# Kernel optimization log

Measured on AMD Instinct MI355X. Metric: run time of the kernel, lower is better.

The kernel has to match this reference:

```python
import jax, jax.numpy as jnp
import numpy as np
from jax import lax

NUM_SELECT = 300
TGT_H, TGT_W = 512, 512  # static resize target; all target_sizes entries equal this


def box_cxcywh_to_xyxy(b):
    cx, cy, w, h = jnp.split(b, 4, axis=-1)
    return jnp.concatenate([cx - 0.5 * w, cy - 0.5 * h, cx + 0.5 * w, cy + 0.5 * h], axis=-1)


def setup_inputs() -> dict:
    key = jax.random.key(0)
    k1, k2, k3, k4 = jax.random.split(key, 4)
    B, Q, C, D, mh, mw = 2, 900, 91, 4, 128, 128
    return {
        "pred_logits": jax.random.normal(k1, (B, Q, C), dtype=jnp.float32),
        "pred_boxes": jax.random.uniform(k2, (B, Q, 4), dtype=jnp.float32),
        "pred_masks": jax.random.normal(k3, (B, Q, mh, mw), dtype=jnp.float32),
        "pred_log_vars": jax.random.normal(k4, (B, Q, D), dtype=jnp.float32),
        "target_sizes": jnp.full((B, 2), TGT_H, dtype=jnp.int32),
    }


def reference(pred_logits, pred_boxes, pred_masks, pred_log_vars, target_sizes):
    B, Q, C = pred_logits.shape
    prob = jax.nn.sigmoid(pred_logits)                      # [B,Q,C]
    topk_values, topk_indexes = lax.top_k(prob.reshape(B, Q * C), NUM_SELECT)
    scores = topk_values                                     # [B,K]
    topk_boxes = topk_indexes // C                           # [B,K] query index
    labels = topk_indexes % C                                # [B,K]

    boxes = box_cxcywh_to_xyxy(pred_boxes)                   # [B,Q,4]
    boxes = jnp.take_along_axis(boxes, topk_boxes[:, :, None], axis=1)  # [B,K,4]

    glv = jnp.take_along_axis(pred_log_vars, topk_boxes[:, :, None], axis=1)  # [B,K,D]
    uncertainty = glv.mean(axis=-1)                          # [B,K]

    ts = target_sizes.astype(boxes.dtype)
    img_h, img_w = ts[:, 0], ts[:, 1]
    scale_fct = jnp.stack([img_w, img_h, img_w, img_h], axis=1)  # [B,4]
    boxes = boxes * scale_fct[:, None, :]

    # gather masks for selected queries, then bilinear resize (align_corners=False)
    sel_masks = jnp.take_along_axis(
        pred_masks, topk_boxes[:, :, None, None], axis=1)    # [B,K,mh,mw]
    mask_logits = jax.image.resize(
        sel_masks, (B, NUM_SELECT, TGT_H, TGT_W), method="bilinear")
    masks = mask_logits > 0.0                                # [B,K,H,W] bool

    return scores, labels, boxes, uncertainty, masks
```

## Files before the change

kernel.cpp:

```cpp
#include <hip/hip_runtime.h>
#include <stdint.h>

#define NSEL 300
#define BB 2
#define QQ 900
#define CC 91
#define NQC (QQ * CC)
#define MH 128
#define MW 128
#define TGT 512

#define NBUCKET 4096
#define CAND_CAP 4096
#define NCHUNK 16
#define CHUNK 5119

typedef float floatx4 __attribute__((ext_vector_type(4)));

#define WS_KEYS   0
#define WS_PART   655360
#define WS_SEL    1179648

__global__ __launch_bounds__(256) void hist_kernel(
    const float* __restrict__ logits, uint8_t* __restrict__ ws)
{
    __shared__ uint32_t hist[NBUCKET];
    const int blk   = blockIdx.x;
    const int b     = blk >> 4;
    const int chunk = blk & 15;

    uint32_t* keys = (uint32_t*)(ws + WS_KEYS) + (size_t)b * NQC;
    uint32_t* part = (uint32_t*)(ws + WS_PART) + (size_t)blk * NBUCKET;

    for (int i = threadIdx.x; i < NBUCKET; i += 256) hist[i] = 0u;
    __syncthreads();

    const int base = chunk * CHUNK;
    int end = base + CHUNK; if (end > NQC) end = NQC;
    const float* lg = logits + (size_t)b * NQC;

    for (int i = base + threadIdx.x; i < end; i += 256) {
        float x = lg[i];
        float p = 1.0f / (1.0f + expf(-x));
        uint32_t key = __float_as_uint(p);
        keys[i] = key;
        atomicAdd(&hist[key >> 18], 1u);
    }
    __syncthreads();

    for (int i = threadIdx.x; i < NBUCKET; i += 256) part[i] = hist[i];
}

__global__ __launch_bounds__(1024) void select_kernel(
    const float* __restrict__ boxes_in,
    const float* __restrict__ logvars,
    const int*   __restrict__ tsizes,
    float* __restrict__ out,
    uint8_t* __restrict__ ws)
{
    __shared__ unsigned long long cand[CAND_CAP];
    __shared__ uint32_t wsum[16];
    __shared__ int s_count;
    __shared__ int s_cut;

    const int b    = blockIdx.x;
    const int tid  = threadIdx.x;
    const int lane = tid & 63;
    const int wid  = tid >> 6;

    if (tid == 0) s_count = 0;

    const uint32_t* part = (const uint32_t*)(ws + WS_PART)
                         + (size_t)b * NCHUNK * NBUCKET;
    uint4 h = make_uint4(0u, 0u, 0u, 0u);
    #pragma unroll
    for (int p = 0; p < NCHUNK; ++p) {
        uint4 v = *(const uint4*)(part + (size_t)p * NBUCKET + 4 * tid);
        h.x += v.x; h.y += v.y; h.z += v.z; h.w += v.w;
    }
    const uint32_t val = h.x + h.y + h.z + h.w;

    uint32_t acc = val;
    #pragma unroll
    for (int off = 1; off < 64; off <<= 1) {
        uint32_t o = __shfl_down(acc, off, 64);
        if (lane + off < 64) acc += o;
    }
    if (lane == 0) wsum[wid] = acc;
    __syncthreads();

    uint32_t later = 0;
    for (int w = wid + 1; w < 16; ++w) later += wsum[w];
    const uint32_t sfx      = acc + later;
    const uint32_t sfx_next = sfx - val;

    if (sfx >= NSEL && sfx_next < NSEL) {
        int a = (int)sfx_next;
        int cut = 4 * tid;
        const uint32_t hh[4] = { h.x, h.y, h.z, h.w };
        for (int k = 3; k >= 0; --k) {
            a += (int)hh[k];
            if (a >= NSEL) { cut = 4 * tid + k; break; }
        }
        s_cut = cut;
    }
    __syncthreads();
    const uint32_t cut = (uint32_t)s_cut;

    const uint32_t* keys = (const uint32_t*)(ws + WS_KEYS) + (size_t)b * NQC;
    for (int i = tid; i < NQC; i += 1024) {
        uint32_t key = keys[i];
        if ((key >> 18) >= cut) {
            int pos = atomicAdd(&s_count, 1);
            if (pos < CAND_CAP) {
                cand[pos] = ((unsigned long long)key << 32)
                          | (uint32_t)(~(uint32_t)i);
            }
        }
    }
    __syncthreads();

    int count = s_count;
    if (count > CAND_CAP) count = CAND_CAP;

    float* out_scores = out;
    float* out_labels = out + 600;
    float* out_boxes  = out + 1200;
    float* out_unc    = out + 3600;
    int*   sel        = (int*)(ws + WS_SEL);

    for (int i = tid; i < count; i += 1024) {
        const unsigned long long my = cand[i];
        int r = 0;
        for (int j = 0; j < count; ++j) r += (cand[j] > my) ? 1 : 0;
        if (r < NSEL) {
            const uint32_t key = (uint32_t)(my >> 32);
            const uint32_t idx = ~((uint32_t)(my & 0xFFFFFFFFull));
            const int q = (int)(idx / CC);
            const int label = (int)(idx - (uint32_t)q * CC);
            const int o = b * NSEL + r;

            out_scores[o] = __uint_as_float(key);
            out_labels[o] = (float)label;

            const float* bx = boxes_in + ((size_t)(b * QQ + q)) * 4;
            float cx = bx[0], cy = bx[1], w = bx[2], hgt = bx[3];
            float hh2 = (float)tsizes[b * 2 + 0];
            float ww2 = (float)tsizes[b * 2 + 1];
            out_boxes[o * 4 + 0] = (cx - 0.5f * w) * ww2;
            out_boxes[o * 4 + 1] = (cy - 0.5f * hgt) * hh2;
            out_boxes[o * 4 + 2] = (cx + 0.5f * w) * ww2;
            out_boxes[o * 4 + 3] = (cy + 0.5f * hgt) * hh2;

            const float* gv = logvars + ((size_t)(b * QQ + q)) * 4;
            float s0 = gv[0] + gv[1];
            float s1 = s0 + gv[2];
            float s2 = s1 + gv[3];
            out_unc[o] = s2 * 0.25f;

            sel[o] = q;
        }
    }
}

__global__ __launch_bounds__(256) void mask_kernel(
    const float* __restrict__ masks_in,
    const int*   __restrict__ sel,
    float* __restrict__ out_masks)
{
    __shared__ float S[18 * MW];

    const int xg = threadIdx.x & 127;
    const int rh = threadIdx.x >> 7;
    const int cm1 = (xg == 0)   ? 0   : xg - 1;
    const int cp1 = (xg == 127) ? 127 : xg + 1;
    const bool eL = (xg == 0);
    const bool eR = (xg == 127);

    const int it0 = 3 * blockIdx.x;
    for (int item = it0; item < it0 + 3; ++item) {
        const int m = item >> 3;
        const int e = item & 7;
        const int b = m / NSEL;
        const int q = sel[m];

        const float* src = masks_in + ((size_t)(b * QQ + q)) * (MH * MW);
        float* dst = out_masks + (size_t)m * (TGT * TGT);

        const int y0   = e * 64;
        const int r_lo = (e == 0) ? 0   : (16 * e - 1);
        const int r_hi = (e == 7) ? 127 : (16 * e + 16);
        const int nrows = r_hi - r_lo + 1;

        {
            const float4* s4 = (const float4*)(src + (size_t)r_lo * MW);
            float4* d4 = (float4*)S;
            const int n4 = nrows * (MW / 4);
            for (int i = threadIdx.x; i < n4; i += 256) d4[i] = s4[i];
        }
        __syncthreads();

        const int k0    = 16 * e + 8 * rh;
        const int rbase = k0 - 1;
        floatx4 h[10];
        #pragma unroll
        for (int j = 0; j < 10; ++j) {
            int r = rbase + j;
            r = (r < 0) ? 0 : (r > MH - 1 ? MH - 1 : r);
            const float* R = S + (r - r_lo) * MW;
            const float a = R[cm1];
            const float c = R[xg];
            const float p = R[cp1];
            floatx4 v;
            v.x = eL ? c : fmaf(0.375f, a, 0.625f * c);
            v.y = eL ? c : fmaf(0.125f, a, 0.875f * c);
            v.z = eR ? c : fmaf(0.125f, p, 0.875f * c);
            v.w = eR ? c : fmaf(0.375f, p, 0.625f * c);
            h[j] = v;
        }

        float* dhalf = dst + (size_t)(y0 + rh * 32) * TGT + 4 * xg;
        #pragma unroll
        for (int g = 0; g < 8; ++g) {
            const floatx4 hA = h[g];
            const floatx4 hB = h[g + 1];
            const floatx4 hC = h[g + 2];
            const floatx4 dAB = hB - hA;
            const floatx4 dBC = hC - hB;

            floatx4 vA, vB, vC, vD;
            #pragma unroll
            for (int u = 0; u < 4; ++u) {
                vA[u] = fmaf(0.625f, dAB[u], hA[u]);
                vB[u] = fmaf(0.875f, dAB[u], hA[u]);
                vC[u] = fmaf(0.125f, dBC[u], hB[u]);
                vD[u] = fmaf(0.375f, dBC[u], hB[u]);
            }
            floatx4 rA, rB, rC, rD;
            #pragma unroll
            for (int u = 0; u < 4; ++u) {
                rA[u] = (vA[u] > 0.0f) ? 1.0f : 0.0f;
                rB[u] = (vB[u] > 0.0f) ? 1.0f : 0.0f;
                rC[u] = (vC[u] > 0.0f) ? 1.0f : 0.0f;
                rD[u] = (vD[u] > 0.0f) ? 1.0f : 0.0f;
            }
            floatx4* p0 = (floatx4*)(dhalf + (size_t)(4 * g    ) * TGT);
            floatx4* p1 = (floatx4*)(dhalf + (size_t)(4 * g + 1) * TGT);
            floatx4* p2 = (floatx4*)(dhalf + (size_t)(4 * g + 2) * TGT);
            floatx4* p3 = (floatx4*)(dhalf + (size_t)(4 * g + 3) * TGT);
            __builtin_nontemporal_store(rA, p0);
            __builtin_nontemporal_store(rB, p1);
            __builtin_nontemporal_store(rC, p2);
            __builtin_nontemporal_store(rD, p3);
        }
        __syncthreads();
    }
}

extern "C" void kernel_launch(void* const* d_in, const int* in_sizes, int n_in,
                              void* d_out, int out_size, void* d_ws, size_t ws_size,
                              hipStream_t stream) {
    (void)in_sizes; (void)n_in; (void)out_size; (void)ws_size;

    const float* pred_logits  = (const float*)d_in[0];
    const float* pred_boxes   = (const float*)d_in[1];
    const float* pred_masks   = (const float*)d_in[2];
    const float* pred_logvars = (const float*)d_in[3];
    const int*   target_sizes = (const int*)d_in[4];

    float*   out = (float*)d_out;
    uint8_t* ws  = (uint8_t*)d_ws;

    hipLaunchKernelGGL(hist_kernel, dim3(BB * NCHUNK), dim3(256), 0, stream,
                       pred_logits, ws);
    hipLaunchKernelGGL(select_kernel, dim3(BB), dim3(1024), 0, stream,
                       pred_boxes, pred_logvars, target_sizes, out, ws);

    float* out_masks = out + 4200;
    const int* sel = (const int*)(ws + WS_SEL);
    hipLaunchKernelGGL(mask_kernel, dim3(1600), dim3(256), 0, stream,
                       pred_masks, sel, out_masks);
}
```

Before: 213.9 us.

## Fuse histogram and top-k selection into one cooperative grid kernel

Replaces the separate histogram and single-block selection kernels with one cooperative kernel of 32 blocks that uses grid syncs between phases. Candidate filtering is now spread over all 32 blocks using global atomics instead of being done by 2 blocks, and one launch boundary is removed. The final ranking is still done by 2 blocks, now with 256 threads each instead of 1024, so that O(count^2) phase has fewer threads. It also adds grid-sync overhead and cooperative launch cost.

```diff
diff --git a/kernel.cpp b/kernel.cpp
--- a/kernel.cpp
+++ b/kernel.cpp
@@ -1,5 +1,8 @@
 #include <hip/hip_runtime.h>
+#include <hip/hip_cooperative_groups.h>
 #include <stdint.h>
+
+namespace cg = cooperative_groups;
 
 #define NSEL 300
 #define BB 2
@@ -17,148 +20,177 @@
 
 typedef float floatx4 __attribute__((ext_vector_type(4)));
 
-#define WS_KEYS   0
-#define WS_PART   655360
-#define WS_SEL    1179648
-
-__global__ __launch_bounds__(256) void hist_kernel(
-    const float* __restrict__ logits, uint8_t* __restrict__ ws)
-{
-    __shared__ uint32_t hist[NBUCKET];
-    const int blk   = blockIdx.x;
-    const int b     = blk >> 4;
-    const int chunk = blk & 15;
-
-    uint32_t* keys = (uint32_t*)(ws + WS_KEYS) + (size_t)b * NQC;
-    uint32_t* part = (uint32_t*)(ws + WS_PART) + (size_t)blk * NBUCKET;
-
-    for (int i = threadIdx.x; i < NBUCKET; i += 256) hist[i] = 0u;
-    __syncthreads();
-
-    const int base = chunk * CHUNK;
-    int end = base + CHUNK; if (end > NQC) end = NQC;
-    const float* lg = logits + (size_t)b * NQC;
-
-    for (int i = base + threadIdx.x; i < end; i += 256) {
-        float x = lg[i];
-        float p = 1.0f / (1.0f + expf(-x));
-        uint32_t key = __float_as_uint(p);
-        keys[i] = key;
-        atomicAdd(&hist[key >> 18], 1u);
-    }
-    __syncthreads();
-
-    for (int i = threadIdx.x; i < NBUCKET; i += 256) part[i] = hist[i];
-}
-
-__global__ __launch_bounds__(1024) void select_kernel(
+#define WS_CAND   0
+#define WS_KEYS   65536
+#define WS_PART   720896
+#define WS_SEL    1245184
+#define WS_CUT    1247584
+#define WS_COUNT  1247592
+
+__global__ __launch_bounds__(256) void topk_coop_kernel(
+    const float* __restrict__ logits,
     const float* __restrict__ boxes_in,
     const float* __restrict__ logvars,
     const int*   __restrict__ tsizes,
     float* __restrict__ out,
     uint8_t* __restrict__ ws)
 {
-    __shared__ unsigned long long cand[CAND_CAP];
-    __shared__ uint32_t wsum[16];
-    __shared__ int s_count;
-    __shared__ int s_cut;
-
-    const int b    = blockIdx.x;
-    const int tid  = threadIdx.x;
-    const int lane = tid & 63;
-    const int wid  = tid >> 6;
-
-    if (tid == 0) s_count = 0;
-
-    const uint32_t* part = (const uint32_t*)(ws + WS_PART)
-                         + (size_t)b * NCHUNK * NBUCKET;
-    uint4 h = make_uint4(0u, 0u, 0u, 0u);
-    #pragma unroll
-    for (int p = 0; p < NCHUNK; ++p) {
-        uint4 v = *(const uint4*)(part + (size_t)p * NBUCKET + 4 * tid);
-        h.x += v.x; h.y += v.y; h.z += v.z; h.w += v.w;
-    }
-    const uint32_t val = h.x + h.y + h.z + h.w;
-
-    uint32_t acc = val;
-    #pragma unroll
-    for (int off = 1; off < 64; off <<= 1) {
-        uint32_t o = __shfl_down(acc, off, 64);
-        if (lane + off < 64) acc += o;
-    }
-    if (lane == 0) wsum[wid] = acc;
-    __syncthreads();
-
-    uint32_t later = 0;
-    for (int w = wid + 1; w < 16; ++w) later += wsum[w];
-    const uint32_t sfx      = acc + later;
-    const uint32_t sfx_next = sfx - val;
-
-    if (sfx >= NSEL && sfx_next < NSEL) {
-        int a = (int)sfx_next;
-        int cut = 4 * tid;
-        const uint32_t hh[4] = { h.x, h.y, h.z, h.w };
-        for (int k = 3; k >= 0; --k) {
-            a += (int)hh[k];
-            if (a >= NSEL) { cut = 4 * tid + k; break; }
-        }
-        s_cut = cut;
-    }
-    __syncthreads();
-    const uint32_t cut = (uint32_t)s_cut;
-
-    const uint32_t* keys = (const uint32_t*)(ws + WS_KEYS) + (size_t)b * NQC;
-    for (int i = tid; i < NQC; i += 1024) {
-        uint32_t key = keys[i];
-        if ((key >> 18) >= cut) {
-            int pos = atomicAdd(&s_count, 1);
-            if (pos < CAND_CAP) {
-                cand[pos] = ((unsigned long long)key << 32)
-                          | (uint32_t)(~(uint32_t)i);
-            }
-        }
-    }
-    __syncthreads();
-
-    int count = s_count;
-    if (count > CAND_CAP) count = CAND_CAP;
-
-    float* out_scores = out;
-    float* out_labels = out + 600;
-    float* out_boxes  = out + 1200;
-    float* out_unc    = out + 3600;
-    int*   sel        = (int*)(ws + WS_SEL);
-
-    for (int i = tid; i < count; i += 1024) {
-        const unsigned long long my = cand[i];
-        int r = 0;
-        for (int j = 0; j < count; ++j) r += (cand[j] > my) ? 1 : 0;
-        if (r < NSEL) {
-            const uint32_t key = (uint32_t)(my >> 32);
-            const uint32_t idx = ~((uint32_t)(my & 0xFFFFFFFFull));
-            const int q = (int)(idx / CC);
-            const int label = (int)(idx - (uint32_t)q * CC);
-            const int o = b * NSEL + r;
-
-            out_scores[o] = __uint_as_float(key);
-            out_labels[o] = (float)label;
-
-            const float* bx = boxes_in + ((size_t)(b * QQ + q)) * 4;
-            float cx = bx[0], cy = bx[1], w = bx[2], hgt = bx[3];
-            float hh2 = (float)tsizes[b * 2 + 0];
-            float ww2 = (float)tsizes[b * 2 + 1];
-            out_boxes[o * 4 + 0] = (cx - 0.5f * w) * ww2;
-            out_boxes[o * 4 + 1] = (cy - 0.5f * hgt) * hh2;
-            out_boxes[o * 4 + 2] = (cx + 0.5f * w) * ww2;
-            out_boxes[o * 4 + 3] = (cy + 0.5f * hgt) * hh2;
-
-            const float* gv = logvars + ((size_t)(b * QQ + q)) * 4;
-            float s0 = gv[0] + gv[1];
-            float s1 = s0 + gv[2];
-            float s2 = s1 + gv[3];
-            out_unc[o] = s2 * 0.25f;
-
-            sel[o] = q;
+    __shared__ unsigned long long scand[CAND_CAP];
+    uint32_t* hist = (uint32_t*)scand;
+    __shared__ uint32_t wsum[4];
+
+    cg::grid_group grid = cg::this_grid();
+
+    const int blk   = blockIdx.x;
+    const int b     = blk >> 4;
+    const int chunk = blk & 15;
+    const int tid   = threadIdx.x;
+    const int lane  = tid & 63;
+    const int wid   = tid >> 6;
+
+    uint32_t* keys_all = (uint32_t*)(ws + WS_KEYS);
+    uint32_t* part_all = (uint32_t*)(ws + WS_PART);
+    uint32_t* cutp     = (uint32_t*)(ws + WS_CUT);
+    int*      countp   = (int*)(ws + WS_COUNT);
+    unsigned long long* cand_all = (unsigned long long*)(ws + WS_CAND);
+
+    {
+        uint32_t* keys = keys_all + (size_t)b * NQC;
+        uint32_t* part = part_all + (size_t)blk * NBUCKET;
+
+        for (int i = tid; i < NBUCKET; i += 256) hist[i] = 0u;
+        __syncthreads();
+
+        const int base = chunk * CHUNK;
+        int end = base + CHUNK; if (end > NQC) end = NQC;
+        const float* lg = logits + (size_t)b * NQC;
+
+        for (int i = base + tid; i < end; i += 256) {
+            float x = lg[i];
+            float p = 1.0f / (1.0f + expf(-x));
+            uint32_t key = __float_as_uint(p);
+            keys[i] = key;
+            atomicAdd(&hist[key >> 18], 1u);
+        }
+        __syncthreads();
+
+        for (int i = tid; i < NBUCKET; i += 256) part[i] = hist[i];
+    }
+    grid.sync();
+
+    if (blk < 2) {
+        const int b2 = blk;
+        const uint32_t* part = part_all + (size_t)b2 * NCHUNK * NBUCKET;
+
+        uint32_t h[16];
+        #pragma unroll
+        for (int j = 0; j < 16; ++j) h[j] = 0u;
+        #pragma unroll
+        for (int p = 0; p < NCHUNK; ++p) {
+            const uint32_t* pp = part + (size_t)p * NBUCKET + 16 * tid;
+            #pragma unroll
+            for (int w = 0; w < 4; ++w) {
+                uint4 v = *(const uint4*)(pp + 4 * w);
+                h[4*w+0] += v.x; h[4*w+1] += v.y; h[4*w+2] += v.z; h[4*w+3] += v.w;
+            }
+        }
+        uint32_t val = 0;
+        #pragma unroll
+        for (int j = 0; j < 16; ++j) val += h[j];
+
+        uint32_t acc = val;
+        #pragma unroll
+        for (int off = 1; off < 64; off <<= 1) {
+            uint32_t o = __shfl_down(acc, off, 64);
+            if (lane + off < 64) acc += o;
+        }
+        if (lane == 0) wsum[wid] = acc;
+        __syncthreads();
+        uint32_t later = 0;
+        for (int w = wid + 1; w < 4; ++w) later += wsum[w];
+        const uint32_t sfx      = acc + later;
+        const uint32_t sfx_next = sfx - val;
+
+        if (sfx >= NSEL && sfx_next < NSEL) {
+            int a = (int)sfx_next;
+            int cut = 16 * tid;
+            for (int k = 15; k >= 0; --k) {
+                a += (int)h[k];
+                if (a >= NSEL) { cut = 16 * tid + k; break; }
+            }
+            cutp[b2]   = (uint32_t)cut;
+            countp[b2] = 0;
+        }
+    }
+    grid.sync();
+
+    {
+        const uint32_t cut = cutp[b];
+        const uint32_t* keys = keys_all + (size_t)b * NQC;
+        unsigned long long* cand = cand_all + (size_t)b * CAND_CAP;
+
+        const int base = chunk * CHUNK;
+        int end = base + CHUNK; if (end > NQC) end = NQC;
+
+        for (int i = base + tid; i < end; i += 256) {
+            uint32_t key = keys[i];
+            if ((key >> 18) >= cut) {
+                int pos = atomicAdd(&countp[b], 1);
+                if (pos < CAND_CAP) {
+                    cand[pos] = ((unsigned long long)key << 32)
+                              | (uint32_t)(~(uint32_t)i);
+                }
+            }
+        }
+    }
+    grid.sync();
+
+    if (blk < 2) {
+        const int b2 = blk;
+        int count = countp[b2];
+        if (count > CAND_CAP) count = CAND_CAP;
+
+        const unsigned long long* gcand = cand_all + (size_t)b2 * CAND_CAP;
+        for (int i = tid; i < count; i += 256) scand[i] = gcand[i];
+        __syncthreads();
+
+        float* out_scores = out;
+        float* out_labels = out + 600;
+        float* out_boxes  = out + 1200;
+        float* out_unc    = out + 3600;
+        int*   sel        = (int*)(ws + WS_SEL);
+
+        for (int i = tid; i < count; i += 256) {
+            const unsigned long long my = scand[i];
+            int r = 0;
+            for (int j = 0; j < count; ++j) r += (scand[j] > my) ? 1 : 0;
+            if (r < NSEL) {
+                const uint32_t key = (uint32_t)(my >> 32);
+                const uint32_t idx = ~((uint32_t)(my & 0xFFFFFFFFull));
+                const int q = (int)(idx / CC);
+                const int label = (int)(idx - (uint32_t)q * CC);
+                const int o = b2 * NSEL + r;
+
+                out_scores[o] = __uint_as_float(key);
+                out_labels[o] = (float)label;
+
+                const float* bx = boxes_in + ((size_t)(b2 * QQ + q)) * 4;
+                float cx = bx[0], cy = bx[1], w = bx[2], hgt = bx[3];
+                float hh2 = (float)tsizes[b2 * 2 + 0];
+                float ww2 = (float)tsizes[b2 * 2 + 1];
+                out_boxes[o * 4 + 0] = (cx - 0.5f * w) * ww2;
+                out_boxes[o * 4 + 1] = (cy - 0.5f * hgt) * hh2;
+                out_boxes[o * 4 + 2] = (cx + 0.5f * w) * ww2;
+                out_boxes[o * 4 + 3] = (cy + 0.5f * hgt) * hh2;
+
+                const float* gv = logvars + ((size_t)(b2 * QQ + q)) * 4;
+                float s0 = gv[0] + gv[1];
+                float s1 = s0 + gv[2];
+                float s2 = s1 + gv[3];
+                out_unc[o] = s2 * 0.25f;
+
+                sel[o] = q;
+            }
         }
     }
 }
@@ -271,10 +303,12 @@
     float*   out = (float*)d_out;
     uint8_t* ws  = (uint8_t*)d_ws;
 
-    hipLaunchKernelGGL(hist_kernel, dim3(BB * NCHUNK), dim3(256), 0, stream,
-                       pred_logits, ws);
-    hipLaunchKernelGGL(select_kernel, dim3(BB), dim3(1024), 0, stream,
-                       pred_boxes, pred_logvars, target_sizes, out, ws);
+    void* args[6] = {
+        (void*)&pred_logits, (void*)&pred_boxes, (void*)&pred_logvars,
+        (void*)&target_sizes, (void*)&out, (void*)&ws
+    };
+    hipLaunchCooperativeKernel((const void*)topk_coop_kernel,
+                               dim3(32), dim3(256), args, 0, stream);
 
     float* out_masks = out + 4200;
     const int* sel = (const int*)(ws + WS_SEL);
```

Measured after the change: 247.6 us. 15.7% more time.
